# Kernel optimization log

Measured on AMD Instinct MI355X. Metric: run time of the kernel, lower is better.

The kernel has to match this reference:

```python
import jax, jax.numpy as jnp
import numpy as np

EPS = 1e-10
TEMP = 1.0


def setup_inputs() -> dict:
    key = jax.random.key(0)
    ks = jax.random.split(key, 8)
    num_nodes, embed_dim, hidden_dim, num_edges = 50000, 128, 64, 600000
    node_embed = jax.random.normal(ks[0], (num_nodes, embed_dim), dtype=jnp.float32)
    edge_index = jax.random.randint(ks[1], (2, num_edges), 0, num_nodes, dtype=jnp.int64)
    u1 = jax.random.uniform(ks[2], (num_edges,), dtype=jnp.float32)
    u2 = jax.random.uniform(ks[3], (num_edges,), dtype=jnp.float32)
    # Linear weights (kaiming-ish scale)
    W1 = jax.random.normal(ks[4], (2 * embed_dim, hidden_dim), dtype=jnp.float32) * (1.0 / np.sqrt(2 * embed_dim))
    b1 = jnp.zeros((hidden_dim,), dtype=jnp.float32)
    W2 = jax.random.normal(ks[5], (hidden_dim, 1), dtype=jnp.float32) * (1.0 / np.sqrt(hidden_dim))
    b2 = jnp.zeros((1,), dtype=jnp.float32)
    return {"node_embed": node_embed, "edge_index": edge_index, "u1": u1, "u2": u2,
            "W1": W1, "b1": b1, "W2": W2, "b2": b2}


def reference(node_embed, edge_index, u1, u2, W1, b1, W2, b2):
    row, col = edge_index[0], edge_index[1]
    # gather + concat: [num_edges, 2*embed_dim]
    edge_feat = jnp.concatenate([node_embed[row], node_embed[col]], axis=1)
    # small MLP (dropout is identity in eval)
    h = jax.nn.relu(edge_feat @ W1 + b1)
    edge_logits = (h @ W2 + b2).squeeze(-1)  # [num_edges]
    # Gumbel-sigmoid (soft)
    g1 = -jnp.log(-jnp.log(jnp.clip(u1, EPS, 1.0 - EPS)))
    g2 = -jnp.log(-jnp.log(jnp.clip(u2, EPS, 1.0 - EPS)))
    edge_probs = jax.nn.sigmoid((edge_logits + g1 - g2) / TEMP)
    return edge_probs
```

## Files before the change

### kernel.cpp

```cpp
#include <hip/hip_runtime.h>
#include <stdint.h>

typedef float  floatx4 __attribute__((ext_vector_type(4)));
typedef short  short8  __attribute__((ext_vector_type(8)));
typedef float  f4v     __attribute__((ext_vector_type(4)));
typedef unsigned int uint32;

#define GS_EPS 1e-10f

__device__ __forceinline__ unsigned short f2bf(float x) {
  uint32 u = __float_as_uint(x);
  u += 0x7FFFu + ((u >> 16) & 1u);
  return (unsigned short)(u >> 16);
}

__global__ void conv_nodes_kernel(const float* __restrict__ src,
                                  unsigned short* __restrict__ dst, int n4) {
  int i = blockIdx.x * 256 + threadIdx.x;
  if (i < n4) {
    f4v v = *(const f4v*)(src + (size_t)i * 4);
    uint32 lo = (uint32)f2bf(v[0]) | ((uint32)f2bf(v[1]) << 16);
    uint32 hi = (uint32)f2bf(v[2]) | ((uint32)f2bf(v[3]) << 16);
    uint32* d = (uint32*)(dst + (size_t)i * 4);
    d[0] = lo;
    d[1] = hi;
  }
}

__global__ void conv_w1_kernel(const float* __restrict__ W1,
                               unsigned short* __restrict__ w1blk) {
  int i = blockIdx.x * 256 + threadIdx.x;
  int chunk = i >> 6;
  int n = i & 63;
  uint32 d[4];
#pragma unroll
  for (int j = 0; j < 4; ++j) {
    unsigned short lo = f2bf(W1[(chunk * 8 + 2 * j) * 64 + n]);
    unsigned short hi = f2bf(W1[(chunk * 8 + 2 * j + 1) * 64 + n]);
    d[j] = (uint32)lo | ((uint32)hi << 16);
  }
  *(uint32*)&w1blk[(size_t)i * 8 + 0] = d[0];
  *(uint32*)&w1blk[(size_t)i * 8 + 2] = d[1];
  *(uint32*)&w1blk[(size_t)i * 8 + 4] = d[2];
  *(uint32*)&w1blk[(size_t)i * 8 + 6] = d[3];
}

#define REDS 272
__global__ __launch_bounds__(512, 6) void edge_mlp_kernel(
    const unsigned short* __restrict__ node_bf16,
    const unsigned short* __restrict__ w1g,
    const int* __restrict__ ei,
    const float* __restrict__ u1, const float* __restrict__ u2,
    const float* __restrict__ b1, const float* __restrict__ W2,
    const float* __restrict__ b2,
    float* __restrict__ out, int num_edges) {
  __shared__ __align__(16) unsigned short w1blk[32 * 64 * 8];
  __shared__ float red[8 * REDS];
  __shared__ float sb1[64];
  __shared__ float sw2[64];
  __shared__ int s_idx64;

  const int tid = threadIdx.x;
  const int wave = tid >> 6;
  const int lane = tid & 63;
  const int q = lane >> 4;
  const int l16 = lane & 15;

  if (tid == 0) s_idx64 = 1;
  __syncthreads();
  if (2 * tid + 1 < 2 * num_edges) {
    if (ei[2 * tid + 1] != 0) s_idx64 = 0;
  }

#pragma unroll
  for (int it = 0; it < 4; ++it) {
    int idx = it * 512 + tid;
    short8 v = *(const short8*)(w1g + (size_t)idx * 8);
    *(short8*)&w1blk[(size_t)idx * 8] = v;
  }
  if (tid < 64) {
    sb1[tid] = b1[tid];
    sw2[tid] = W2[tid];
  }
  __syncthreads();
  const bool idx64 = (s_idx64 != 0);

  const int wavebase = blockIdx.x * 256 + wave * 32;

  int nr[2], nc[2];
#pragma unroll
  for (int mt = 0; mt < 2; ++mt) {
    int e = wavebase + mt * 16 + l16;
    if (e > num_edges - 1) e = num_edges - 1;
    if (idx64) {
      nr[mt] = ei[2 * e];
      nc[mt] = ei[2 * (num_edges + e)];
    } else {
      nr[mt] = ei[e];
      nc[mt] = ei[num_edges + e];
    }
  }

  floatx4 acc[2][4];
#pragma unroll
  for (int mt = 0; mt < 2; ++mt)
#pragma unroll
    for (int nn = 0; nn < 4; ++nn) {
      floatx4 z = {0.f, 0.f, 0.f, 0.f};
      acc[mt][nn] = z;
    }

  short8 acur[2], anxt[2];
#pragma unroll
  for (int mt = 0; mt < 2; ++mt)
    acur[mt] = *(const short8*)(node_bf16 + (size_t)nr[mt] * 128 + q * 8);

#pragma unroll
  for (int kk = 0; kk < 8; ++kk) {
    if (kk < 7) {
      int kn = kk + 1;
      int off = (kn & 3) * 32 + q * 8;
#pragma unroll
      for (int mt = 0; mt < 2; ++mt) {
        int node = (kn < 4) ? nr[mt] : nc[mt];
        anxt[mt] = *(const short8*)(node_bf16 + (size_t)node * 128 + off);
      }
    }
    short8 bf[4];
#pragma unroll
    for (int nn = 0; nn < 4; ++nn)
      bf[nn] = *(const short8*)&w1blk[(size_t)((kk * 4 + q) * 64 + nn * 16 + l16) * 8];
#pragma unroll
    for (int mt = 0; mt < 2; ++mt)
#pragma unroll
      for (int nn = 0; nn < 4; ++nn)
        acc[mt][nn] = __builtin_amdgcn_mfma_f32_16x16x32_bf16(acur[mt], bf[nn],
                                                              acc[mt][nn], 0, 0, 0);
    acur[0] = anxt[0];
    acur[1] = anxt[1];
  }

  float b1v[4], w2v[4];
#pragma unroll
  for (int nn = 0; nn < 4; ++nn) {
    int n = nn * 16 + l16;
    b1v[nn] = sb1[n];
    w2v[nn] = sw2[n];
  }
  const float bias2 = b2[0];

  float* rw = &red[wave * REDS];
  float logitA = 0.f, logitB = 0.f;
#pragma unroll
  for (int mt = 0; mt < 2; ++mt) {
    float p[4];
#pragma unroll
    for (int r = 0; r < 4; ++r) p[r] = 0.f;
#pragma unroll
    for (int nn = 0; nn < 4; ++nn) {
      floatx4 a = acc[mt][nn];
      float bb = b1v[nn], ww = w2v[nn];
      p[0] += fmaxf(a[0] + bb, 0.f) * ww;
      p[1] += fmaxf(a[1] + bb, 0.f) * ww;
      p[2] += fmaxf(a[2] + bb, 0.f) * ww;
      p[3] += fmaxf(a[3] + bb, 0.f) * ww;
    }
#pragma unroll
    for (int r = 0; r < 4; ++r) rw[(q * 4 + r) * 17 + l16] = p[r];
    float s = rw[l16 * 17 + q * 4 + 0] + rw[l16 * 17 + q * 4 + 1] +
              rw[l16 * 17 + q * 4 + 2] + rw[l16 * 17 + q * 4 + 3];
    s += __shfl_xor(s, 16, 64);
    s += __shfl_xor(s, 32, 64);
    if (mt == 0) logitA = s; else logitB = s;
  }

  if (lane < 32) {
    float logit = ((lane < 16) ? logitA : logitB) + bias2;
    int e = wavebase + lane;
    if (e < num_edges) {
      float a1 = fminf(fmaxf(u1[e], GS_EPS), 1.0f);
      float a2 = fminf(fmaxf(u2[e], GS_EPS), 1.0f);
      float g1 = -__logf(-__logf(a1));
      float g2 = -__logf(-__logf(a2));
      float x = logit + g1 - g2;
      out[e] = 1.f / (1.f + __expf(-x));
    }
  }
}

extern "C" void kernel_launch(void* const* d_in, const int* in_sizes, int n_in,
                              void* d_out, int out_size, void* d_ws, size_t ws_size,
                              hipStream_t stream) {
  const float* node_embed = (const float*)d_in[0];
  const int* ei = (const int*)d_in[1];
  const float* u1 = (const float*)d_in[2];
  const float* u2 = (const float*)d_in[3];
  const float* W1 = (const float*)d_in[4];
  const float* b1 = (const float*)d_in[5];
  const float* W2 = (const float*)d_in[6];
  const float* b2 = (const float*)d_in[7];
  float* out = (float*)d_out;

  const int num_edges = in_sizes[2];
  const int num_nodes = in_sizes[0] / 128;

  unsigned short* node_bf16 = (unsigned short*)d_ws;
  const size_t node_tbl_bytes = (size_t)num_nodes * 128 * sizeof(unsigned short);
  unsigned short* w1blk = (unsigned short*)((char*)d_ws + ((node_tbl_bytes + 15) & ~(size_t)15));

  int n4 = (num_nodes * 128) / 4;
  conv_nodes_kernel<<<(n4 + 255) / 256, 256, 0, stream>>>(node_embed, node_bf16, n4);
  conv_w1_kernel<<<8, 256, 0, stream>>>(W1, w1blk);

  const int nblocks = (num_edges + 255) / 256;
  edge_mlp_kernel<<<nblocks, 512, 0, stream>>>(
      node_bf16, w1blk, ei, u1, u2, b1, W2, b2, out, num_edges);
}
```

Baseline: 136.1 us.

## Halve edges per wave, issue all gathers upfront, shuffle-reduce logits, widen conversion

Each wave now handles 16 edges instead of 32, and all eight node-row gathers are issued before the barrier so they overlap the W1 staging into shared memory, replacing the one-step software prefetch. The LDS reduction buffer and the block-wide index-width detection are dropped in favour of a per-wave ballot and xor-shuffle reductions, and launch bounds are raised to allow more resident blocks. The node conversion kernel now writes 16-byte bf16 stores. The cost is twice as many blocks, each reloading W1 into LDS, and higher register pressure from holding all A fragments at once.

```diff
diff --git a/kernel.cpp b/kernel.cpp
--- a/kernel.cpp
+++ b/kernel.cpp
@@ -15,15 +15,17 @@
 }
 
 __global__ void conv_nodes_kernel(const float* __restrict__ src,
-                                  unsigned short* __restrict__ dst, int n4) {
+                                  unsigned short* __restrict__ dst, int n8) {
   int i = blockIdx.x * 256 + threadIdx.x;
-  if (i < n4) {
-    f4v v = *(const f4v*)(src + (size_t)i * 4);
-    uint32 lo = (uint32)f2bf(v[0]) | ((uint32)f2bf(v[1]) << 16);
-    uint32 hi = (uint32)f2bf(v[2]) | ((uint32)f2bf(v[3]) << 16);
-    uint32* d = (uint32*)(dst + (size_t)i * 4);
-    d[0] = lo;
-    d[1] = hi;
+  if (i < n8) {
+    f4v v0 = *(const f4v*)(src + (size_t)i * 8);
+    f4v v1 = *(const f4v*)(src + (size_t)i * 8 + 4);
+    short8 t;
+    t[0] = (short)f2bf(v0[0]); t[1] = (short)f2bf(v0[1]);
+    t[2] = (short)f2bf(v0[2]); t[3] = (short)f2bf(v0[3]);
+    t[4] = (short)f2bf(v1[0]); t[5] = (short)f2bf(v1[1]);
+    t[6] = (short)f2bf(v1[2]); t[7] = (short)f2bf(v1[3]);
+    *(short8*)(dst + (size_t)i * 8) = t;
   }
 }
 
@@ -45,8 +47,7 @@
   *(uint32*)&w1blk[(size_t)i * 8 + 6] = d[3];
 }
 
-#define REDS 272
-__global__ __launch_bounds__(512, 6) void edge_mlp_kernel(
+__global__ __launch_bounds__(512, 8) void edge_mlp_kernel(
     const unsigned short* __restrict__ node_bf16,
     const unsigned short* __restrict__ w1g,
     const int* __restrict__ ei,
@@ -55,22 +56,13 @@
     const float* __restrict__ b2,
     float* __restrict__ out, int num_edges) {
   __shared__ __align__(16) unsigned short w1blk[32 * 64 * 8];
-  __shared__ float red[8 * REDS];
-  __shared__ float sb1[64];
-  __shared__ float sw2[64];
-  __shared__ int s_idx64;
 
   const int tid = threadIdx.x;
   const int wave = tid >> 6;
   const int lane = tid & 63;
   const int q = lane >> 4;
   const int l16 = lane & 15;
-
-  if (tid == 0) s_idx64 = 1;
-  __syncthreads();
-  if (2 * tid + 1 < 2 * num_edges) {
-    if (ei[2 * tid + 1] != 0) s_idx64 = 0;
-  }
+  const int wavebase = blockIdx.x * 128 + wave * 16;
 
 #pragma unroll
   for (int it = 0; it < 4; ++it) {
@@ -78,112 +70,80 @@
     short8 v = *(const short8*)(w1g + (size_t)idx * 8);
     *(short8*)&w1blk[(size_t)idx * 8] = v;
   }
-  if (tid < 64) {
-    sb1[tid] = b1[tid];
-    sw2[tid] = W2[tid];
+
+  int el = wavebase + lane;
+  if (el > num_edges - 1) el = num_edges - 1;
+  unsigned long long oddmask = __ballot(ei[2 * el + 1] != 0);
+  const bool idx64 = (oddmask == 0ULL);
+
+  int e = wavebase + l16;
+  if (e > num_edges - 1) e = num_edges - 1;
+  int nr, nc;
+  if (idx64) {
+    nr = ei[2 * e];
+    nc = ei[2 * (num_edges + e)];
+  } else {
+    nr = ei[e];
+    nc = ei[num_edges + e];
   }
+
+  short8 af[8];
+  {
+    const unsigned short* pr = node_bf16 + (size_t)nr * 128 + q * 8;
+    const unsigned short* pc = node_bf16 + (size_t)nc * 128 + q * 8;
+#pragma unroll
+    for (int kk = 0; kk < 4; ++kk) af[kk] = *(const short8*)(pr + kk * 32);
+#pragma unroll
+    for (int kk = 0; kk < 4; ++kk) af[4 + kk] = *(const short8*)(pc + kk * 32);
+  }
+
   __syncthreads();
-  const bool idx64 = (s_idx64 != 0);
 
-  const int wavebase = blockIdx.x * 256 + wave * 32;
+  floatx4 acc[4];
+#pragma unroll
+  for (int nn = 0; nn < 4; ++nn) {
+    floatx4 z = {0.f, 0.f, 0.f, 0.f};
+    acc[nn] = z;
+  }
 
-  int nr[2], nc[2];
 #pragma unroll
-  for (int mt = 0; mt < 2; ++mt) {
-    int e = wavebase + mt * 16 + l16;
-    if (e > num_edges - 1) e = num_edges - 1;
-    if (idx64) {
-      nr[mt] = ei[2 * e];
-      nc[mt] = ei[2 * (num_edges + e)];
-    } else {
-      nr[mt] = ei[e];
-      nc[mt] = ei[num_edges + e];
+  for (int kk = 0; kk < 8; ++kk) {
+#pragma unroll
+    for (int nn = 0; nn < 4; ++nn) {
+      short8 bf = *(const short8*)&w1blk[(size_t)((kk * 4 + q) * 64 + nn * 16 + l16) * 8];
+      acc[nn] = __builtin_amdgcn_mfma_f32_16x16x32_bf16(af[kk], bf, acc[nn], 0, 0, 0);
     }
   }
 
-  floatx4 acc[2][4];
-#pragma unroll
-  for (int mt = 0; mt < 2; ++mt)
-#pragma unroll
-    for (int nn = 0; nn < 4; ++nn) {
-      floatx4 z = {0.f, 0.f, 0.f, 0.f};
-      acc[mt][nn] = z;
-    }
-
-  short8 acur[2], anxt[2];
-#pragma unroll
-  for (int mt = 0; mt < 2; ++mt)
-    acur[mt] = *(const short8*)(node_bf16 + (size_t)nr[mt] * 128 + q * 8);
-
-#pragma unroll
-  for (int kk = 0; kk < 8; ++kk) {
-    if (kk < 7) {
-      int kn = kk + 1;
-      int off = (kn & 3) * 32 + q * 8;
-#pragma unroll
-      for (int mt = 0; mt < 2; ++mt) {
-        int node = (kn < 4) ? nr[mt] : nc[mt];
-        anxt[mt] = *(const short8*)(node_bf16 + (size_t)node * 128 + off);
-      }
-    }
-    short8 bf[4];
-#pragma unroll
-    for (int nn = 0; nn < 4; ++nn)
-      bf[nn] = *(const short8*)&w1blk[(size_t)((kk * 4 + q) * 64 + nn * 16 + l16) * 8];
-#pragma unroll
-    for (int mt = 0; mt < 2; ++mt)
-#pragma unroll
-      for (int nn = 0; nn < 4; ++nn)
-        acc[mt][nn] = __builtin_amdgcn_mfma_f32_16x16x32_bf16(acur[mt], bf[nn],
-                                                              acc[mt][nn], 0, 0, 0);
-    acur[0] = anxt[0];
-    acur[1] = anxt[1];
-  }
-
-  float b1v[4], w2v[4];
+  float p0 = 0.f, p1 = 0.f, p2 = 0.f, p3 = 0.f;
 #pragma unroll
   for (int nn = 0; nn < 4; ++nn) {
-    int n = nn * 16 + l16;
-    b1v[nn] = sb1[n];
-    w2v[nn] = sw2[n];
+    float bb = b1[nn * 16 + l16];
+    float ww = W2[nn * 16 + l16];
+    floatx4 a = acc[nn];
+    p0 += fmaxf(a[0] + bb, 0.f) * ww;
+    p1 += fmaxf(a[1] + bb, 0.f) * ww;
+    p2 += fmaxf(a[2] + bb, 0.f) * ww;
+    p3 += fmaxf(a[3] + bb, 0.f) * ww;
   }
-  const float bias2 = b2[0];
-
-  float* rw = &red[wave * REDS];
-  float logitA = 0.f, logitB = 0.f;
 #pragma unroll
-  for (int mt = 0; mt < 2; ++mt) {
-    float p[4];
-#pragma unroll
-    for (int r = 0; r < 4; ++r) p[r] = 0.f;
-#pragma unroll
-    for (int nn = 0; nn < 4; ++nn) {
-      floatx4 a = acc[mt][nn];
-      float bb = b1v[nn], ww = w2v[nn];
-      p[0] += fmaxf(a[0] + bb, 0.f) * ww;
-      p[1] += fmaxf(a[1] + bb, 0.f) * ww;
-      p[2] += fmaxf(a[2] + bb, 0.f) * ww;
-      p[3] += fmaxf(a[3] + bb, 0.f) * ww;
-    }
-#pragma unroll
-    for (int r = 0; r < 4; ++r) rw[(q * 4 + r) * 17 + l16] = p[r];
-    float s = rw[l16 * 17 + q * 4 + 0] + rw[l16 * 17 + q * 4 + 1] +
-              rw[l16 * 17 + q * 4 + 2] + rw[l16 * 17 + q * 4 + 3];
-    s += __shfl_xor(s, 16, 64);
-    s += __shfl_xor(s, 32, 64);
-    if (mt == 0) logitA = s; else logitB = s;
+  for (int s = 1; s < 16; s <<= 1) {
+    p0 += __shfl_xor(p0, s, 64);
+    p1 += __shfl_xor(p1, s, 64);
+    p2 += __shfl_xor(p2, s, 64);
+    p3 += __shfl_xor(p3, s, 64);
   }
-
-  if (lane < 32) {
-    float logit = ((lane < 16) ? logitA : logitB) + bias2;
-    int e = wavebase + lane;
-    if (e < num_edges) {
-      float a1 = fminf(fmaxf(u1[e], GS_EPS), 1.0f);
-      float a2 = fminf(fmaxf(u2[e], GS_EPS), 1.0f);
+  if (l16 < 4) {
+    float logit = (l16 == 0) ? p0 : (l16 == 1) ? p1 : (l16 == 2) ? p2 : p3;
+    logit += b2[0];
+    int eo = wavebase + q * 4 + l16;
+    if (eo < num_edges) {
+      float a1 = fminf(fmaxf(u1[eo], GS_EPS), 1.0f);
+      float a2 = fminf(fmaxf(u2[eo], GS_EPS), 1.0f);
       float g1 = -__logf(-__logf(a1));
       float g2 = -__logf(-__logf(a2));
       float x = logit + g1 - g2;
-      out[e] = 1.f / (1.f + __expf(-x));
+      out[eo] = 1.f / (1.f + __expf(-x));
     }
   }
 }
@@ -208,11 +168,11 @@
   const size_t node_tbl_bytes = (size_t)num_nodes * 128 * sizeof(unsigned short);
   unsigned short* w1blk = (unsigned short*)((char*)d_ws + ((node_tbl_bytes + 15) & ~(size_t)15));
 
-  int n4 = (num_nodes * 128) / 4;
-  conv_nodes_kernel<<<(n4 + 255) / 256, 256, 0, stream>>>(node_embed, node_bf16, n4);
+  int n8 = (num_nodes * 128) / 8;
+  conv_nodes_kernel<<<(n8 + 255) / 256, 256, 0, stream>>>(node_embed, node_bf16, n8);
   conv_w1_kernel<<<8, 256, 0, stream>>>(W1, w1blk);
 
-  const int nblocks = (num_edges + 255) / 256;
+  const int nblocks = (num_edges + 127) / 128;
   edge_mlp_kernel<<<nblocks, 512, 0, stream>>>(
       node_bf16, w1blk, ei, u1, u2, b1, W2, b2, out, num_edges);
 }
```

After: 135.7 us. Within noise of the previous version (-0.3%).
